# Kernel optimization log

Hardware: AMD Instinct MI355X
Metric: run time of the kernel (lower is better)

## Reference

```python
import jax, jax.numpy as jnp
import numpy as np

EMBED = 128
HEADS = 8
HEAD_DIM = EMBED // HEADS


def setup_inputs() -> dict:
    key = jax.random.key(0)
    ks = jax.random.split(key, 11)
    B, T, N, C = 8, 64, 170, EMBED
    s = 1.0 / np.sqrt(C)
    return {
        "values": jax.random.normal(ks[0], (B, T, N, C), dtype=jnp.float32),
        "keys": jax.random.normal(ks[1], (B, T, N, C), dtype=jnp.float32),
        "query": jax.random.normal(ks[2], (B, T, N, C), dtype=jnp.float32),
        "Wv": jax.random.normal(ks[3], (C, C), dtype=jnp.float32) * s,
        "bv": jnp.zeros((C,), dtype=jnp.float32),
        "Wk": jax.random.normal(ks[4], (C, C), dtype=jnp.float32) * s,
        "bk": jnp.zeros((C,), dtype=jnp.float32),
        "Wq": jax.random.normal(ks[5], (C, C), dtype=jnp.float32) * s,
        "bq": jnp.zeros((C,), dtype=jnp.float32),
        "Wo": jax.random.normal(ks[6], (C, C), dtype=jnp.float32) * s,
        "bo": jnp.zeros((C,), dtype=jnp.float32),
    }


def reference(values, keys, query, Wv, bv, Wk, bk, Wq, bq, Wo, bo):
    B, T, N, C = query.shape
    H, D = HEADS, HEAD_DIM
    # Linear projections (torch nn.Linear: x @ W.T + b)
    v = (values @ Wv.T + bv).reshape(B, T, N, H, D)
    k = (keys @ Wk.T + bk).reshape(B, T, N, H, D)
    q = (query @ Wq.T + bq).reshape(B, T, N, H, D)
    # spatial mode: attention over nodes N, independent per (b, t, h)
    energy = jnp.einsum('btqhd,btkhd->btqkh', q, k)  # [B,T,N,N,H]
    scale = jnp.asarray(C, q.dtype) ** 0.5
    attn = jax.nn.softmax(energy / scale, axis=3)
    out = jnp.einsum('btqkh,btkhd->btqhd', attn, v).reshape(B, T, N, H * D)
    return out @ Wo.T + bo
```

## Files before the change

### kernel.cpp

```cpp
#include <hip/hip_runtime.h>
#include <cstdint>

typedef float   f32x4  __attribute__((ext_vector_type(4)));
typedef __bf16  bf16x4 __attribute__((ext_vector_type(4)));
typedef __bf16  bf16x8 __attribute__((ext_vector_type(8)));

#if __has_builtin(__builtin_amdgcn_exp2f)
#define EXP2F(x) __builtin_amdgcn_exp2f(x)
#else
#define EXP2F(x) exp2f(x)
#endif

#define BT_TOTAL 512
#define NNODES 170
#define CDIM 128
#define HEADS 8
#define HDIM 16
#define SLAB (NNODES*HDIM)
#define NPAD 176
#define VSLAB (HDIM*NPAD)
#define QKV_ELEMS ((size_t)BT_TOTAL*HEADS*SLAB)
#define WPAD 136
#define S2L2E 0.12753851f

__global__ __launch_bounds__(256) void wconv_kernel(const float* __restrict__ wq,
                                                    const float* __restrict__ wk,
                                                    const float* __restrict__ wv,
                                                    const float* __restrict__ wo,
                                                    __bf16* __restrict__ wbf) {
    int idx = blockIdx.x * 256 + threadIdx.x;
    if (idx >= 4 * 16384) return;
    int mat = idx >> 14, rem = idx & 16383;
    int c = rem >> 7, o = rem & 127;
    int kk = o >> 5, l4 = (o & 31) >> 3, j = o & 7;
    int col = kk * 32 + l4 * 4 + (j & 3) + 16 * (j >> 2);
    const float* W = (mat == 0) ? wq : (mat == 1) ? wk : (mat == 2) ? wv : wo;
    float scale = (mat == 0) ? S2L2E : 1.0f;
    wbf[idx] = (__bf16)(W[c * 128 + col] * scale);
}

__global__ __launch_bounds__(256, 4) void qkv_kernel(const float* __restrict__ qin,
    const float* __restrict__ kin, const float* __restrict__ vin,
    const __bf16* __restrict__ wbf,
    const float* __restrict__ bq, const float* __restrict__ bk, const float* __restrict__ bv,
    __bf16* __restrict__ qws, __bf16* __restrict__ kws, __bf16* __restrict__ vt) {
    __shared__ __bf16 Wl[128 * WPAD];
    int t = threadIdx.x;
    int iid = blockIdx.x / BT_TOTAL;
    int bt  = blockIdx.x % BT_TOTAL;
    const float* X    = (iid == 0) ? qin : (iid == 1) ? kin : vin;
    const float* bias = (iid == 0) ? bq  : (iid == 1) ? bk  : bv;
    float wscale = (iid == 0) ? S2L2E : 1.0f;
    const __bf16* wb = wbf + iid * 16384;
    #pragma unroll
    for (int i = 0; i < 8; ++i) {
        int idx = i * 256 + t;
        int c = idx >> 4, x = (idx & 15) * 8;
        *(bf16x8*)&Wl[c * WPAD + x] = *(const bf16x8*)&wb[idx * 8];
    }
    __syncthreads();

    int w = t >> 6, lane = t & 63, li = lane & 15, l4 = lane >> 4;
    const f32x4 zf = {0.f, 0.f, 0.f, 0.f};

    auto loadA = [&](f32x4* A, int tile) {
        int mrow = tile * 16 + li;
        bool v = mrow < NNODES;
        const float* xr = X + ((size_t)(bt * NNODES + mrow)) * CDIM;
        #pragma unroll
        for (int kk = 0; kk < 4; ++kk) {
            A[2 * kk]     = v ? *(const f32x4*)(xr + kk * 32 + l4 * 4)      : zf;
            A[2 * kk + 1] = v ? *(const f32x4*)(xr + kk * 32 + l4 * 4 + 16) : zf;
        }
    };
    auto compute = [&](const f32x4* A, int tile) {
        f32x4 acc[8] = {};
        #pragma unroll
        for (int kk = 0; kk < 4; ++kk) {
            f32x4 a0 = A[2 * kk], a1 = A[2 * kk + 1];
            bf16x8 a = { (__bf16)a0[0], (__bf16)a0[1], (__bf16)a0[2], (__bf16)a0[3],
                         (__bf16)a1[0], (__bf16)a1[1], (__bf16)a1[2], (__bf16)a1[3] };
            #pragma unroll
            for (int nt = 0; nt < 8; ++nt) {
                bf16x8 b = *(const bf16x8*)&Wl[(nt * 16 + li) * WPAD + kk * 32 + l4 * 8];
                if (iid < 2)
                    acc[nt] = __builtin_amdgcn_mfma_f32_16x16x32_bf16(b, a, acc[nt], 0, 0, 0);
                else
                    acc[nt] = __builtin_amdgcn_mfma_f32_16x16x32_bf16(a, b, acc[nt], 0, 0, 0);
            }
        }
        if (iid < 2) {
            __bf16* dst = ((iid == 0) ? qws : kws) + (size_t)bt * HEADS * SLAB;
            int n = tile * 16 + li;
            if (n < NNODES) {
                #pragma unroll
                for (int nt = 0; nt < 8; ++nt) {
                    f32x4 b4 = *(const f32x4*)&bias[nt * 16 + l4 * 4];
                    f32x4 ov = acc[nt] + b4 * wscale;
                    bf16x4 o4 = { (__bf16)ov[0], (__bf16)ov[1], (__bf16)ov[2], (__bf16)ov[3] };
                    *(bf16x4*)&dst[(size_t)nt * SLAB + n * HDIM + l4 * 4] = o4;
                }
            }
        } else {
            __bf16* dst = vt + (size_t)bt * HEADS * VSLAB;
            int n0 = tile * 16 + l4 * 4;
            #pragma unroll
            for (int nt = 0; nt < 8; ++nt) {
                float bval = bias[nt * 16 + li];
                __bf16* d2 = dst + (size_t)nt * VSLAB + li * NPAD + n0;
                if (n0 + 3 < NNODES) {
                    bf16x4 o4 = { (__bf16)(acc[nt][0] + bval), (__bf16)(acc[nt][1] + bval),
                                  (__bf16)(acc[nt][2] + bval), (__bf16)(acc[nt][3] + bval) };
                    *(bf16x4*)d2 = o4;
                } else {
                    #pragma unroll
                    for (int r = 0; r < 4; ++r)
                        if (n0 + r < NNODES) d2[r] = (__bf16)(acc[nt][r] + bval);
                }
            }
        }
    };

    f32x4 A0[8], A1[8];
    loadA(A0, w);
    loadA(A1, w + 4);
    compute(A0, w);
    if (w < 3) loadA(A0, w + 8);
    compute(A1, w + 4);
    if (w < 3) compute(A0, w + 8);
}

__global__ __launch_bounds__(256) void attn_kernel(const __bf16* __restrict__ qws,
                                                   const __bf16* __restrict__ kws,
                                                   const __bf16* __restrict__ vt,
                                                   __bf16* __restrict__ ows) {
    int unit = blockIdx.x * 4 + (threadIdx.x >> 6);
    int half = unit & 1, bh = unit >> 1;
    int bt = bh >> 3, h = bh & 7;
    int lane = threadIdx.x & 63, li = lane & 15, l4 = lane >> 4;
    const __bf16* qb  = qws + ((size_t)(bt * HEADS + h)) * SLAB;
    const __bf16* kb  = kws + ((size_t)(bt * HEADS + h)) * SLAB;
    const __bf16* vtb = vt  + ((size_t)(bt * HEADS + h)) * VSLAB;
    __bf16* ob = ows + (size_t)bt * NNODES * CDIM + (h >> 1) * 32 + (h & 1) * 4;
    const __bf16 bz = (__bf16)0.0f;
    const bf16x4 z4 = {bz, bz, bz, bz};
    const f32x4 zf = {0.f, 0.f, 0.f, 0.f};

    bf16x4 kf[11];
    #pragma unroll
    for (int tt = 0; tt < 11; ++tt)
        kf[tt] = *(const bf16x4*)&kb[(tt * 16 + li) * HDIM + l4 * 4];

    bf16x8 vf[6];
    #pragma unroll
    for (int s = 0; s < 5; ++s) {
        bf16x4 a = *(const bf16x4*)&vtb[li * NPAD + 32 * s + 4 * l4];
        bf16x4 b = *(const bf16x4*)&vtb[li * NPAD + 32 * s + 4 * l4 + 16];
        vf[s] = __builtin_shufflevector(a, b, 0, 1, 2, 3, 4, 5, 6, 7);
    }
    {
        bf16x4 a = *(const bf16x4*)&vtb[li * NPAD + 160 + 4 * l4];
        bf16x8 v5 = { (160 + 4 * l4 + 0 < NNODES) ? a[0] : bz,
                      (160 + 4 * l4 + 1 < NNODES) ? a[1] : bz,
                      (160 + 4 * l4 + 2 < NNODES) ? a[2] : bz,
                      (160 + 4 * l4 + 3 < NNODES) ? a[3] : bz,
                      bz, bz, bz, bz };
        vf[5] = v5;
    }

    int q0 = half ? 6 : 0;
    int qn = half ? 5 : 6;
    for (int qi = 0; qi < qn; ++qi) {
        int qc = q0 + qi;
        bf16x4 qv = *(const bf16x4*)&qb[(qc * 16 + li) * HDIM + l4 * 4];
        bf16x8 qf = __builtin_shufflevector(qv, z4, 0, 1, 2, 3, 4, 5, 6, 7);
        bf16x4 ph[11];
        f32x4 s4 = zf;
        #pragma unroll
        for (int tt = 0; tt < 11; ++tt) {
            bf16x8 a = __builtin_shufflevector(kf[tt], z4, 0, 1, 2, 3, 4, 5, 6, 7);
            f32x4 e = __builtin_amdgcn_mfma_f32_16x16x32_bf16(a, qf, zf, 0, 0, 0);
            if (tt == 10) {
                #pragma unroll
                for (int r = 0; r < 4; ++r)
                    e[r] = (160 + l4 * 4 + r < NNODES) ? e[r] : -1.0e30f;
            }
            f32x4 p;
            p[0] = EXP2F(e[0]); p[1] = EXP2F(e[1]);
            p[2] = EXP2F(e[2]); p[3] = EXP2F(e[3]);
            s4 += p;
            ph[tt] = __builtin_convertvector(p, bf16x4);
        }
        float sum = (s4[0] + s4[1]) + (s4[2] + s4[3]);
        sum += __shfl_xor(sum, 16);
        sum += __shfl_xor(sum, 32);
        float inv = 1.0f / sum;
        f32x4 o0 = zf, o1 = zf;
        o0 = __builtin_amdgcn_mfma_f32_16x16x32_bf16(vf[0],
                __builtin_shufflevector(ph[0], ph[1], 0,1,2,3,4,5,6,7), o0, 0,0,0);
        o1 = __builtin_amdgcn_mfma_f32_16x16x32_bf16(vf[1],
                __builtin_shufflevector(ph[2], ph[3], 0,1,2,3,4,5,6,7), o1, 0,0,0);
        o0 = __builtin_amdgcn_mfma_f32_16x16x32_bf16(vf[2],
                __builtin_shufflevector(ph[4], ph[5], 0,1,2,3,4,5,6,7), o0, 0,0,0);
        o1 = __builtin_amdgcn_mfma_f32_16x16x32_bf16(vf[3],
                __builtin_shufflevector(ph[6], ph[7], 0,1,2,3,4,5,6,7), o1, 0,0,0);
        o0 = __builtin_amdgcn_mfma_f32_16x16x32_bf16(vf[4],
                __builtin_shufflevector(ph[8], ph[9], 0,1,2,3,4,5,6,7), o0, 0,0,0);
        o1 = __builtin_amdgcn_mfma_f32_16x16x32_bf16(vf[5],
                __builtin_shufflevector(ph[10], z4,    0,1,2,3,4,5,6,7), o1, 0,0,0);
        f32x4 o = (o0 + o1) * inv;
        int q = qc * 16 + li;
        if (q < NNODES) {
            bf16x4 ov = { (__bf16)o[0], (__bf16)o[1], (__bf16)o[2], (__bf16)o[3] };
            *(bf16x4*)&ob[(size_t)q * CDIM + l4 * 8] = ov;
        }
    }
}

__global__ __launch_bounds__(512) void oproj_kernel(const __bf16* __restrict__ ows,
                                                    const __bf16* __restrict__ wbf,
                                                    const float* __restrict__ bo,
                                                    float* __restrict__ out) {
    __shared__ __bf16 Wl[128 * WPAD];
    int t = threadIdx.x;
    int bt = blockIdx.x;
    const __bf16* wo = wbf + 3 * 16384;
    #pragma unroll
    for (int i = 0; i < 4; ++i) {
        int idx = i * 512 + t;
        int c = idx >> 4, x = (idx & 15) * 8;
        *(bf16x8*)&Wl[c * WPAD + x] = *(const bf16x8*)&wo[idx * 8];
    }
    __syncthreads();

    int w = t >> 6, lane = t & 63, li = lane & 15, l4 = lane >> 4;
    const bf16x8 z8 = {};

    auto loadO = [&](bf16x8* A, int tile) {
        int mrow = tile * 16 + li;
        bool v = mrow < NNODES;
        const __bf16* ar = ows + ((size_t)(bt * NNODES + mrow)) * CDIM;
        #pragma unroll
        for (int kk = 0; kk < 4; ++kk)
            A[kk] = v ? *(const bf16x8*)(ar + kk * 32 + l4 * 8) : z8;
    };
    auto computeO = [&](const bf16x8* A, int tile) {
        f32x4 acc[8] = {};
        #pragma unroll
        for (int kk = 0; kk < 4; ++kk) {
            #pragma unroll
            for (int nt = 0; nt < 8; ++nt) {
                bf16x8 b = *(const bf16x8*)&Wl[(nt * 16 + li) * WPAD + kk * 32 + l4 * 8];
                acc[nt] = __builtin_amdgcn_mfma_f32_16x16x32_bf16(b, A[kk], acc[nt], 0, 0, 0);
            }
        }
        int n = tile * 16 + li;
        if (n < NNODES) {
            float* orow = out + ((size_t)bt * NNODES + n) * CDIM;
            #pragma unroll
            for (int nt = 0; nt < 8; ++nt) {
                f32x4 b4 = *(const f32x4*)&bo[nt * 16 + l4 * 4];
                *(f32x4*)&orow[nt * 16 + l4 * 4] = acc[nt] + b4;
            }
        }
    };

    bf16x8 A0[4], A1[4];
    loadO(A0, w);
    if (w < 3) loadO(A1, w + 8);
    computeO(A0, w);
    if (w < 3) computeO(A1, w + 8);
}

extern "C" void kernel_launch(void* const* d_in, const int* in_sizes, int n_in,
                              void* d_out, int out_size, void* d_ws, size_t ws_size,
                              hipStream_t stream) {
    const float* values = (const float*)d_in[0];
    const float* keys   = (const float*)d_in[1];
    const float* query  = (const float*)d_in[2];
    const float* Wv = (const float*)d_in[3];
    const float* bv = (const float*)d_in[4];
    const float* Wk = (const float*)d_in[5];
    const float* bk = (const float*)d_in[6];
    const float* Wq = (const float*)d_in[7];
    const float* bq = (const float*)d_in[8];
    const float* Wo = (const float*)d_in[9];
    const float* bo = (const float*)d_in[10];
    float* out = (float*)d_out;

    __bf16* qws = (__bf16*)d_ws;
    __bf16* kws = qws + QKV_ELEMS;
    __bf16* ows = kws + QKV_ELEMS;
    __bf16* wbf = ows + QKV_ELEMS;
    __bf16* vt  = (__bf16*)d_out;

    hipLaunchKernelGGL(wconv_kernel, dim3(256),  dim3(256), 0, stream, Wq, Wk, Wv, Wo, wbf);
    hipLaunchKernelGGL(qkv_kernel,   dim3(1536), dim3(256), 0, stream,
                       query, keys, values, wbf, bq, bk, bv, qws, kws, vt);
    hipLaunchKernelGGL(attn_kernel,  dim3(2048), dim3(256), 0, stream, qws, kws, vt, ows);
    hipLaunchKernelGGL(oproj_kernel, dim3(512),  dim3(512), 0, stream, ows, wbf, bo, out);
}
```

Measured before the change: 103.5 us.

## Hold QKV weights in registers, convert Wo in oproj, simplify masking and layout

The QKV projection kernel now loads its bf16 weight fragments straight from global memory into registers, dropping the LDS staging and the barrier. The oproj kernel converts fp32 Wo to bf16 in shared memory itself, so wconv no longer handles Wo, and its output uses nontemporal stores. The attention kernel writes its output in natural head-major layout, masks padded keys with a multiply after exp instead of a select before it, and delays normalisation until the store. The V padding shrinks, and the extra register pressure in the QKV kernel may lower occupancy.

```diff
diff --git a/kernel.cpp b/kernel.cpp
--- a/kernel.cpp
+++ b/kernel.cpp
@@ -17,51 +17,47 @@
 #define HEADS 8
 #define HDIM 16
 #define SLAB (NNODES*HDIM)
-#define NPAD 176
+#define NPAD 172
 #define VSLAB (HDIM*NPAD)
 #define QKV_ELEMS ((size_t)BT_TOTAL*HEADS*SLAB)
-#define WPAD 136
 #define S2L2E 0.12753851f
 
 __global__ __launch_bounds__(256) void wconv_kernel(const float* __restrict__ wq,
                                                     const float* __restrict__ wk,
                                                     const float* __restrict__ wv,
-                                                    const float* __restrict__ wo,
                                                     __bf16* __restrict__ wbf) {
     int idx = blockIdx.x * 256 + threadIdx.x;
-    if (idx >= 4 * 16384) return;
+    if (idx >= 3 * 16384) return;
     int mat = idx >> 14, rem = idx & 16383;
     int c = rem >> 7, o = rem & 127;
     int kk = o >> 5, l4 = (o & 31) >> 3, j = o & 7;
     int col = kk * 32 + l4 * 4 + (j & 3) + 16 * (j >> 2);
-    const float* W = (mat == 0) ? wq : (mat == 1) ? wk : (mat == 2) ? wv : wo;
+    const float* W = (mat == 0) ? wq : (mat == 1) ? wk : wv;
     float scale = (mat == 0) ? S2L2E : 1.0f;
     wbf[idx] = (__bf16)(W[c * 128 + col] * scale);
 }
 
-__global__ __launch_bounds__(256, 4) void qkv_kernel(const float* __restrict__ qin,
+__global__ __launch_bounds__(256) void qkv_kernel(const float* __restrict__ qin,
     const float* __restrict__ kin, const float* __restrict__ vin,
     const __bf16* __restrict__ wbf,
     const float* __restrict__ bq, const float* __restrict__ bk, const float* __restrict__ bv,
     __bf16* __restrict__ qws, __bf16* __restrict__ kws, __bf16* __restrict__ vt) {
-    __shared__ __bf16 Wl[128 * WPAD];
-    int t = threadIdx.x;
-    int iid = blockIdx.x / BT_TOTAL;
-    int bt  = blockIdx.x % BT_TOTAL;
+    int bid = blockIdx.x;
+    int iid = bid / BT_TOTAL;
+    int bt  = bid % BT_TOTAL;
     const float* X    = (iid == 0) ? qin : (iid == 1) ? kin : vin;
     const float* bias = (iid == 0) ? bq  : (iid == 1) ? bk  : bv;
     float wscale = (iid == 0) ? S2L2E : 1.0f;
+    int t = threadIdx.x, w = t >> 6, lane = t & 63, li = lane & 15, l4 = lane >> 4;
+    const f32x4 zf = {0.f, 0.f, 0.f, 0.f};
+
     const __bf16* wb = wbf + iid * 16384;
-    #pragma unroll
-    for (int i = 0; i < 8; ++i) {
-        int idx = i * 256 + t;
-        int c = idx >> 4, x = (idx & 15) * 8;
-        *(bf16x8*)&Wl[c * WPAD + x] = *(const bf16x8*)&wb[idx * 8];
-    }
-    __syncthreads();
-
-    int w = t >> 6, lane = t & 63, li = lane & 15, l4 = lane >> 4;
-    const f32x4 zf = {0.f, 0.f, 0.f, 0.f};
+    bf16x8 wf[8][4];
+    #pragma unroll
+    for (int nt = 0; nt < 8; ++nt)
+        #pragma unroll
+        for (int kk = 0; kk < 4; ++kk)
+            wf[nt][kk] = *(const bf16x8*)&wb[(nt * 16 + li) * 128 + kk * 32 + l4 * 8];
 
     auto loadA = [&](f32x4* A, int tile) {
         int mrow = tile * 16 + li;
@@ -82,11 +78,10 @@
                          (__bf16)a1[0], (__bf16)a1[1], (__bf16)a1[2], (__bf16)a1[3] };
             #pragma unroll
             for (int nt = 0; nt < 8; ++nt) {
-                bf16x8 b = *(const bf16x8*)&Wl[(nt * 16 + li) * WPAD + kk * 32 + l4 * 8];
                 if (iid < 2)
-                    acc[nt] = __builtin_amdgcn_mfma_f32_16x16x32_bf16(b, a, acc[nt], 0, 0, 0);
+                    acc[nt] = __builtin_amdgcn_mfma_f32_16x16x32_bf16(wf[nt][kk], a, acc[nt], 0, 0, 0);
                 else
-                    acc[nt] = __builtin_amdgcn_mfma_f32_16x16x32_bf16(a, b, acc[nt], 0, 0, 0);
+                    acc[nt] = __builtin_amdgcn_mfma_f32_16x16x32_bf16(a, wf[nt][kk], acc[nt], 0, 0, 0);
             }
         }
         if (iid < 2) {
@@ -114,8 +109,8 @@
                     *(bf16x4*)d2 = o4;
                 } else {
                     #pragma unroll
-                    for (int r = 0; r < 4; ++r)
-                        if (n0 + r < NNODES) d2[r] = (__bf16)(acc[nt][r] + bval);
+                    for (int rr = 0; rr < 4; ++rr)
+                        if (n0 + rr < NNODES) d2[rr] = (__bf16)(acc[nt][rr] + bval);
                 }
             }
         }
@@ -141,7 +136,7 @@
     const __bf16* qb  = qws + ((size_t)(bt * HEADS + h)) * SLAB;
     const __bf16* kb  = kws + ((size_t)(bt * HEADS + h)) * SLAB;
     const __bf16* vtb = vt  + ((size_t)(bt * HEADS + h)) * VSLAB;
-    __bf16* ob = ows + (size_t)bt * NNODES * CDIM + (h >> 1) * 32 + (h & 1) * 4;
+    __bf16* ob = ows + (size_t)bt * NNODES * CDIM + h * HDIM;
     const __bf16 bz = (__bf16)0.0f;
     const bf16x4 z4 = {bz, bz, bz, bz};
     const f32x4 zf = {0.f, 0.f, 0.f, 0.f};
@@ -167,6 +162,10 @@
                       bz, bz, bz, bz };
         vf[5] = v5;
     }
+    f32x4 mk = { (160 + l4 * 4 + 0 < NNODES) ? 1.f : 0.f,
+                 (160 + l4 * 4 + 1 < NNODES) ? 1.f : 0.f,
+                 (160 + l4 * 4 + 2 < NNODES) ? 1.f : 0.f,
+                 (160 + l4 * 4 + 3 < NNODES) ? 1.f : 0.f };
 
     int q0 = half ? 6 : 0;
     int qn = half ? 5 : 6;
@@ -180,14 +179,10 @@
         for (int tt = 0; tt < 11; ++tt) {
             bf16x8 a = __builtin_shufflevector(kf[tt], z4, 0, 1, 2, 3, 4, 5, 6, 7);
             f32x4 e = __builtin_amdgcn_mfma_f32_16x16x32_bf16(a, qf, zf, 0, 0, 0);
-            if (tt == 10) {
-                #pragma unroll
-                for (int r = 0; r < 4; ++r)
-                    e[r] = (160 + l4 * 4 + r < NNODES) ? e[r] : -1.0e30f;
-            }
             f32x4 p;
             p[0] = EXP2F(e[0]); p[1] = EXP2F(e[1]);
             p[2] = EXP2F(e[2]); p[3] = EXP2F(e[3]);
+            if (tt == 10) p *= mk;
             s4 += p;
             ph[tt] = __builtin_convertvector(p, bf16x4);
         }
@@ -208,68 +203,68 @@
                 __builtin_shufflevector(ph[8], ph[9], 0,1,2,3,4,5,6,7), o0, 0,0,0);
         o1 = __builtin_amdgcn_mfma_f32_16x16x32_bf16(vf[5],
                 __builtin_shufflevector(ph[10], z4,    0,1,2,3,4,5,6,7), o1, 0,0,0);
-        f32x4 o = (o0 + o1) * inv;
+        f32x4 o = o0 + o1;
         int q = qc * 16 + li;
         if (q < NNODES) {
-            bf16x4 ov = { (__bf16)o[0], (__bf16)o[1], (__bf16)o[2], (__bf16)o[3] };
-            *(bf16x4*)&ob[(size_t)q * CDIM + l4 * 8] = ov;
+            bf16x4 ov = { (__bf16)(o[0] * inv), (__bf16)(o[1] * inv),
+                          (__bf16)(o[2] * inv), (__bf16)(o[3] * inv) };
+            *(bf16x4*)&ob[(size_t)q * CDIM + l4 * 4] = ov;
         }
     }
 }
 
 __global__ __launch_bounds__(512) void oproj_kernel(const __bf16* __restrict__ ows,
-                                                    const __bf16* __restrict__ wbf,
+                                                    const float* __restrict__ Wo,
                                                     const float* __restrict__ bo,
                                                     float* __restrict__ out) {
-    __shared__ __bf16 Wl[128 * WPAD];
+    __shared__ __bf16 Wl[128 * 132];
     int t = threadIdx.x;
     int bt = blockIdx.x;
-    const __bf16* wo = wbf + 3 * 16384;
-    #pragma unroll
-    for (int i = 0; i < 4; ++i) {
+    #pragma unroll
+    for (int i = 0; i < 8; ++i) {
         int idx = i * 512 + t;
-        int c = idx >> 4, x = (idx & 15) * 8;
-        *(bf16x8*)&Wl[c * WPAD + x] = *(const bf16x8*)&wo[idx * 8];
+        int r = idx >> 5, c = (idx & 31) * 4;
+        f32x4 w4 = *(const f32x4*)&Wo[r * 128 + c];
+        bf16x4 wb = { (__bf16)w4[0], (__bf16)w4[1], (__bf16)w4[2], (__bf16)w4[3] };
+        *(bf16x4*)&Wl[r * 132 + c] = wb;
     }
     __syncthreads();
 
     int w = t >> 6, lane = t & 63, li = lane & 15, l4 = lane >> 4;
-    const bf16x8 z8 = {};
-
-    auto loadO = [&](bf16x8* A, int tile) {
-        int mrow = tile * 16 + li;
-        bool v = mrow < NNODES;
-        const __bf16* ar = ows + ((size_t)(bt * NNODES + mrow)) * CDIM;
-        #pragma unroll
-        for (int kk = 0; kk < 4; ++kk)
-            A[kk] = v ? *(const bf16x8*)(ar + kk * 32 + l4 * 8) : z8;
-    };
-    auto computeO = [&](const bf16x8* A, int tile) {
+    const bf16x4 z4 = {(__bf16)0.f, (__bf16)0.f, (__bf16)0.f, (__bf16)0.f};
+    for (int mt = 0; mt < 2; ++mt) {
+        int tbase = mt * 128 + w * 16;
+        if (tbase >= NNODES) break;
+        int mrow = tbase + li;
+        bool mvalid = mrow < NNODES;
+        const __bf16* arow = ows + ((size_t)bt * NNODES + mrow) * CDIM;
         f32x4 acc[8] = {};
         #pragma unroll
         for (int kk = 0; kk < 4; ++kk) {
-            #pragma unroll
-            for (int nt = 0; nt < 8; ++nt) {
-                bf16x8 b = *(const bf16x8*)&Wl[(nt * 16 + li) * WPAD + kk * 32 + l4 * 8];
-                acc[nt] = __builtin_amdgcn_mfma_f32_16x16x32_bf16(b, A[kk], acc[nt], 0, 0, 0);
-            }
-        }
-        int n = tile * 16 + li;
+            int kb = kk * 32 + l4 * 4;
+            bf16x4 a0 = mvalid ? *(const bf16x4*)(arow + kb)      : z4;
+            bf16x4 a1 = mvalid ? *(const bf16x4*)(arow + kb + 16) : z4;
+            bf16x8 a = __builtin_shufflevector(a0, a1, 0, 1, 2, 3, 4, 5, 6, 7);
+            #pragma unroll
+            for (int nt = 0; nt < 8; ++nt) {
+                int c = nt * 16 + li;
+                bf16x4 b0 = *(const bf16x4*)&Wl[c * 132 + kb];
+                bf16x4 b1 = *(const bf16x4*)&Wl[c * 132 + kb + 16];
+                bf16x8 b = __builtin_shufflevector(b0, b1, 0, 1, 2, 3, 4, 5, 6, 7);
+                acc[nt] = __builtin_amdgcn_mfma_f32_16x16x32_bf16(b, a, acc[nt], 0, 0, 0);
+            }
+        }
+        int n = tbase + li;
         if (n < NNODES) {
             float* orow = out + ((size_t)bt * NNODES + n) * CDIM;
             #pragma unroll
             for (int nt = 0; nt < 8; ++nt) {
                 f32x4 b4 = *(const f32x4*)&bo[nt * 16 + l4 * 4];
-                *(f32x4*)&orow[nt * 16 + l4 * 4] = acc[nt] + b4;
-            }
-        }
-    };
-
-    bf16x8 A0[4], A1[4];
-    loadO(A0, w);
-    if (w < 3) loadO(A1, w + 8);
-    computeO(A0, w);
-    if (w < 3) computeO(A1, w + 8);
+                f32x4 o = acc[nt] + b4;
+                __builtin_nontemporal_store(o, (f32x4*)&orow[nt * 16 + l4 * 4]);
+            }
+        }
+    }
 }
 
 extern "C" void kernel_launch(void* const* d_in, const int* in_sizes, int n_in,
@@ -294,9 +289,9 @@
     __bf16* wbf = ows + QKV_ELEMS;
     __bf16* vt  = (__bf16*)d_out;
 
-    hipLaunchKernelGGL(wconv_kernel, dim3(256),  dim3(256), 0, stream, Wq, Wk, Wv, Wo, wbf);
+    hipLaunchKernelGGL(wconv_kernel, dim3(192),  dim3(256), 0, stream, Wq, Wk, Wv, wbf);
     hipLaunchKernelGGL(qkv_kernel,   dim3(1536), dim3(256), 0, stream,
                        query, keys, values, wbf, bq, bk, bv, qws, kws, vt);
     hipLaunchKernelGGL(attn_kernel,  dim3(2048), dim3(256), 0, stream, qws, kws, vt, ows);
-    hipLaunchKernelGGL(oproj_kernel, dim3(512),  dim3(512), 0, stream, ows, wbf, bo, out);
-}
+    hipLaunchKernelGGL(oproj_kernel, dim3(512),  dim3(512), 0, stream, ows, Wo, bo, out);
+}
```

Measured after the change: 134.0 us. +29.5%, slower.
